# Optimization experiments

Measured on AMD Instinct MI355X. Metric: run time of the kernel, lower is better.

Reference implementation:

```python
import jax, jax.numpy as jnp
import numpy as np

B, H, W, A, C = 32, 64, 64, 5, 80
D = 5 + C  # per-anchor block


def setup_inputs() -> dict:
    key = jax.random.key(0)
    k1, k2, k3, k4 = jax.random.split(key, 4)
    model_output = jax.random.normal(k1, (B, H, W, A * D), jnp.float32) * 0.1
    # label: coords/classes in [0,1), wh offsets small, conf channel strictly 0 or 1
    lab = jax.random.uniform(k2, (B, H, W, A, D), jnp.float32)
    conf = (jax.random.uniform(k3, (B, H, W, A)) < 0.05).astype(jnp.float32)
    wh = jax.random.normal(k4, (B, H, W, A, 2), jnp.float32) * 0.3
    lab = lab.at[..., 2:4].set(wh).at[..., 4].set(conf)
    label = lab.reshape(B, H, W, A * D)
    original_img_sizes = jnp.full((B, 2), 416.0, jnp.float32)  # [h, w] per image
    anchor_boxes = jnp.array([[30.0, 25.0], [60.0, 55.0], [110.0, 95.0],
                              [180.0, 160.0], [300.0, 280.0]], jnp.float32)  # [A,2] = [h,w]
    return {"model_output": model_output, "label": label,
            "original_img_sizes": original_img_sizes, "anchor_boxes": anchor_boxes}


def _smooth_l1(x):
    ax = jnp.abs(x)
    return jnp.where(ax < 1.0, 0.5 * x * x, ax - 0.5)


def _yolo_loss(model_output, label, original_img_sizes, anchor_boxes,
               lamda_coord, lamda_noobj, lamda_obj, lamda_class):
    b, h, w, ch = model_output.shape
    a = anchor_boxes.shape[0]
    d = ch // a
    out = model_output.reshape(b, h, w, a, d)
    lab = label.reshape(b, h, w, a, d)

    obj = lab[..., 4] >= 1.0            # [B,H,W,A]
    noobj = lab[..., 4] == 0.0
    objf = obj.astype(out.dtype)
    noobjf = noobj.astype(out.dtype)

    xg = jnp.arange(w, dtype=out.dtype)[None, None, :, None]   # x grid index
    yg = jnp.arange(h, dtype=out.dtype)[None, :, None, None]   # y grid index
    ylen = (original_img_sizes[:, 0] / h)[:, None, None, None]
    xlen = (original_img_sizes[:, 1] / w)[:, None, None, None]
    aw = anchor_boxes[:, 1]  # broadcast over A axis
    ah = anchor_boxes[:, 0]

    # predicted box decode (NB: pred ymax uses x_center -- faithful to source bug)
    pxc = (xg + out[..., 0]) * xlen
    pyc = (yg + out[..., 1]) * ylen
    pw = jnp.exp(out[..., 2]) * aw
    ph = jnp.exp(out[..., 3]) * ah
    pxmin, pxmax = pxc - pw / 2, pxc + pw / 2
    pymin, pymax = pyc - ph / 2, pxc + ph / 2  # source bug: x_center here

    # true box decode
    txc = (xg + lab[..., 0]) * xlen
    tyc = (yg + lab[..., 1]) * ylen
    tw = jnp.exp(lab[..., 2]) * aw
    th = jnp.exp(lab[..., 3]) * ah
    txmin, txmax = txc - tw / 2, txc + tw / 2
    tymin, tymax = tyc - th / 2, tyc + th / 2

    iw = jnp.maximum(jnp.minimum(pxmax, txmax) - jnp.maximum(pxmin, txmin), 0.0)
    ih = jnp.maximum(jnp.minimum(pymax, tymax) - jnp.maximum(pymin, tymin), 0.0)
    inter = iw * ih
    area_p = (pxmax - pxmin) * (pymax - pymin)
    area_t = (txmax - txmin) * (tymax - tymin)
    union = area_p + area_t - inter
    iou = inter / jnp.where(obj, union, 1.0)
    iou = jnp.where(obj, iou, 0.0)      # ious tensor is zero at non-obj cells

    new_conf = lab[..., 4] * iou        # label conf channel *= ious

    p1 = (objf * ((out[..., :2] - lab[..., :2]) ** 2).sum(-1)).sum()
    p2 = (objf * _smooth_l1(out[..., 2:4] - lab[..., 2:4]).sum(-1)).sum()
    p3 = (objf * (out[..., 4] - new_conf) ** 2).sum()
    p4 = (noobjf * (out[..., 4] - new_conf) ** 2).sum()
    p5 = (objf * ((out[..., 5:] - lab[..., 5:]) ** 2).sum(-1)).sum()

    return (lamda_coord * p1 + lamda_coord * p2 + lamda_obj * p3
            + lamda_noobj * p4 + lamda_class * p5)


def reference(model_output, label, original_img_sizes, anchor_boxes,
              lamda_coord=5.0, lamda_noobj=0.5, lamda_obj=1.0, lamda_class=1.0):
    return _yolo_loss(model_output, label, original_img_sizes, anchor_boxes,
                      lamda_coord, lamda_noobj, lamda_obj, lamda_class)
```

## Files before the change

### kernel.cpp

```cpp
#include <hip/hip_runtime.h>


constexpr int Bc = 32, Hc = 64, Wc = 64, Ac = 5, Dc = 85, Cc = 80;
constexpr int NCELL = Bc * Hc * Wc * Ac;
constexpr float LAMDA_COORD = 5.0f;
constexpr float LAMDA_NOOBJ = 0.5f;
constexpr float LAMDA_OBJ   = 1.0f;
constexpr float LAMDA_CLASS = 1.0f;

__global__ void zero_kernel(float* out) {
    if (threadIdx.x == 0 && blockIdx.x == 0) out[0] = 0.0f;
}

__device__ __forceinline__ float smooth_l1(float x) {
    float ax = fabsf(x);
    return (ax < 1.0f) ? 0.5f * x * x : ax - 0.5f;
}

__global__ __launch_bounds__(256) void yolo_loss_kernel(
    const float* __restrict__ mo,
    const float* __restrict__ lb,
    const float* __restrict__ orig,
    const float* __restrict__ anch,
    float* __restrict__ result)
{
    int idx = blockIdx.x * blockDim.x + threadIdx.x;
    float loss = 0.0f;

    if (idx < NCELL) {
        long base = (long)idx * Dc;
        float lab4 = lb[base + 4];
        float out4 = mo[base + 4];

        if (lab4 == 0.0f) {
            loss = LAMDA_NOOBJ * out4 * out4;
        } else if (lab4 >= 1.0f) {
            int a = idx % Ac;
            int t = idx / Ac;
            int w = t % Wc; t /= Wc;
            int h = t % Hc;
            int b = t / Hc;

            float o0 = mo[base + 0], o1 = mo[base + 1];
            float o2 = mo[base + 2], o3 = mo[base + 3];
            float l0 = lb[base + 0], l1 = lb[base + 1];
            float l2 = lb[base + 2], l3 = lb[base + 3];

            float ylen = orig[b * 2 + 0] * (1.0f / Hc);
            float xlen = orig[b * 2 + 1] * (1.0f / Wc);
            float aw = anch[a * 2 + 1];
            float ah = anch[a * 2 + 0];

            float pxc = ((float)w + o0) * xlen;
            float pyc = ((float)h + o1) * ylen;
            float pw  = __expf(o2) * aw;
            float ph  = __expf(o3) * ah;
            float pxmin = pxc - pw * 0.5f, pxmax = pxc + pw * 0.5f;
            float pymin = pyc - ph * 0.5f;
            float pymax = pxc + ph * 0.5f;

            float txc = ((float)w + l0) * xlen;
            float tyc = ((float)h + l1) * ylen;
            float tw  = __expf(l2) * aw;
            float th  = __expf(l3) * ah;
            float txmin = txc - tw * 0.5f, txmax = txc + tw * 0.5f;
            float tymin = tyc - th * 0.5f, tymax = tyc + th * 0.5f;

            float iw = fmaxf(fminf(pxmax, txmax) - fmaxf(pxmin, txmin), 0.0f);
            float ih = fmaxf(fminf(pymax, tymax) - fmaxf(pymin, tymin), 0.0f);
            float inter  = iw * ih;
            float area_p = (pxmax - pxmin) * (pymax - pymin);
            float area_t = (txmax - txmin) * (tymax - tymin);
            float uni    = area_p + area_t - inter;
            float iou    = inter / uni;
            float new_conf = lab4 * iou;

            float d0 = o0 - l0, d1 = o1 - l1;
            float p1 = d0 * d0 + d1 * d1;
            float p2 = smooth_l1(o2 - l2) + smooth_l1(o3 - l3);
            float dc = out4 - new_conf;
            float p3 = dc * dc;

            float p5 = 0.0f;
            #pragma unroll 8
            for (int c = 0; c < Cc; ++c) {
                float d = mo[base + 5 + c] - lb[base + 5 + c];
                p5 += d * d;
            }

            loss = LAMDA_COORD * (p1 + p2) + LAMDA_OBJ * p3 + LAMDA_CLASS * p5;
        }
    }

    #pragma unroll
    for (int off = 32; off > 0; off >>= 1)
        loss += __shfl_down(loss, off);

    __shared__ float smem[4];
    int lane = threadIdx.x & 63;
    int wid  = threadIdx.x >> 6;
    if (lane == 0) smem[wid] = loss;
    __syncthreads();
    if (threadIdx.x == 0) {
        float tot = smem[0] + smem[1] + smem[2] + smem[3];
        atomicAdd(result, tot);
    }
}

extern "C" void kernel_launch(void* const* d_in, const int* in_sizes, int n_in,
                              void* d_out, int out_size, void* d_ws, size_t ws_size,
                              hipStream_t stream) {
    const float* mo   = (const float*)d_in[0];
    const float* lb   = (const float*)d_in[1];
    const float* orig = (const float*)d_in[2];
    const float* anch = (const float*)d_in[3];
    float* result = (float*)d_out;

    zero_kernel<<<1, 64, 0, stream>>>(result);

    int block = 256;
    int grid = (NCELL + block - 1) / block;
    yolo_loss_kernel<<<grid, block, 0, stream>>>(mo, lb, orig, anch, result);
}
```

Measured before the change: 60.69 us.

## Compact object cells in shared memory and process each with a full wavefront

Each thread now only checks the confidence channel and handles the no-object case itself. Object cells are appended to a shared-memory list, and each wavefront then handles one listed cell at a time: lanes load the 85 channels in a coalesced way, and the class loss is reduced with shuffles. This replaces strided per-thread loops over 80 class channels, which are uncoalesced and divergent, at the cost of extra barriers, a shared atomic, and shuffle reductions.

```diff
diff --git a/kernel.cpp b/kernel.cpp
--- a/kernel.cpp
+++ b/kernel.cpp
@@ -1,7 +1,7 @@
 #include <hip/hip_runtime.h>
 
 
-constexpr int Bc = 32, Hc = 64, Wc = 64, Ac = 5, Dc = 85, Cc = 80;
+constexpr int Bc = 32, Hc = 64, Wc = 64, Ac = 5, Dc = 85;
 constexpr int NCELL = Bc * Hc * Wc * Ac;
 constexpr float LAMDA_COORD = 5.0f;
 constexpr float LAMDA_NOOBJ = 0.5f;
@@ -24,85 +24,109 @@
     const float* __restrict__ anch,
     float* __restrict__ result)
 {
-    int idx = blockIdx.x * blockDim.x + threadIdx.x;
+    const int tid  = threadIdx.x;
+    const int lane = tid & 63;
+    const int wid  = tid >> 6;
+    const int idx  = blockIdx.x * 256 + tid;
+
+    __shared__ int   s_objidx[256];
+    __shared__ int   s_cnt;
+    __shared__ float s_partial[4];
+    if (tid == 0) s_cnt = 0;
+    __syncthreads();
+
     float loss = 0.0f;
 
-    if (idx < NCELL) {
+    {
         long base = (long)idx * Dc;
         float lab4 = lb[base + 4];
         float out4 = mo[base + 4];
-
         if (lab4 == 0.0f) {
             loss = LAMDA_NOOBJ * out4 * out4;
         } else if (lab4 >= 1.0f) {
-            int a = idx % Ac;
-            int t = idx / Ac;
-            int w = t % Wc; t /= Wc;
-            int h = t % Hc;
-            int b = t / Hc;
+            int p = atomicAdd(&s_cnt, 1);
+            s_objidx[p] = idx;
+        }
+    }
+    __syncthreads();
+    const int n = s_cnt;
 
-            float o0 = mo[base + 0], o1 = mo[base + 1];
-            float o2 = mo[base + 2], o3 = mo[base + 3];
-            float l0 = lb[base + 0], l1 = lb[base + 1];
-            float l2 = lb[base + 2], l3 = lb[base + 3];
+    for (int i = wid; i < n; i += 4) {
+        const int cidx = s_objidx[i];
+        const long base = (long)cidx * Dc;
 
-            float ylen = orig[b * 2 + 0] * (1.0f / Hc);
-            float xlen = orig[b * 2 + 1] * (1.0f / Wc);
-            float aw = anch[a * 2 + 1];
-            float ah = anch[a * 2 + 0];
+        float o_a = mo[base + lane];
+        float l_a = lb[base + lane];
+        float o_b = 0.0f, l_b = 0.0f;
+        if (lane < Dc - 64) {
+            o_b = mo[base + 64 + lane];
+            l_b = lb[base + 64 + lane];
+        }
 
-            float pxc = ((float)w + o0) * xlen;
-            float pyc = ((float)h + o1) * ylen;
-            float pw  = __expf(o2) * aw;
-            float ph  = __expf(o3) * ah;
-            float pxmin = pxc - pw * 0.5f, pxmax = pxc + pw * 0.5f;
-            float pymin = pyc - ph * 0.5f;
-            float pymax = pxc + ph * 0.5f;
+        float da = (lane >= 5) ? (o_a - l_a) : 0.0f;
+        float db = o_b - l_b;
+        float p5 = da * da + db * db;
+        #pragma unroll
+        for (int off = 32; off > 0; off >>= 1)
+            p5 += __shfl_down(p5, off);
 
-            float txc = ((float)w + l0) * xlen;
-            float tyc = ((float)h + l1) * ylen;
-            float tw  = __expf(l2) * aw;
-            float th  = __expf(l3) * ah;
-            float txmin = txc - tw * 0.5f, txmax = txc + tw * 0.5f;
-            float tymin = tyc - th * 0.5f, tymax = tyc + th * 0.5f;
+        float o0 = __shfl(o_a, 0), o1 = __shfl(o_a, 1), o2 = __shfl(o_a, 2),
+              o3 = __shfl(o_a, 3), o4 = __shfl(o_a, 4);
+        float l0 = __shfl(l_a, 0), l1 = __shfl(l_a, 1), l2 = __shfl(l_a, 2),
+              l3 = __shfl(l_a, 3), l4 = __shfl(l_a, 4);
 
-            float iw = fmaxf(fminf(pxmax, txmax) - fmaxf(pxmin, txmin), 0.0f);
-            float ih = fmaxf(fminf(pymax, tymax) - fmaxf(pymin, tymin), 0.0f);
-            float inter  = iw * ih;
-            float area_p = (pxmax - pxmin) * (pymax - pymin);
-            float area_t = (txmax - txmin) * (tymax - tymin);
-            float uni    = area_p + area_t - inter;
-            float iou    = inter / uni;
-            float new_conf = lab4 * iou;
+        int a = cidx % Ac;
+        int t = cidx / Ac;
+        int w = t & (Wc - 1); t >>= 6;
+        int h = t & (Hc - 1);
+        int b = t >> 6;
 
-            float d0 = o0 - l0, d1 = o1 - l1;
-            float p1 = d0 * d0 + d1 * d1;
-            float p2 = smooth_l1(o2 - l2) + smooth_l1(o3 - l3);
-            float dc = out4 - new_conf;
-            float p3 = dc * dc;
+        float ylen = orig[b * 2 + 0] * (1.0f / Hc);
+        float xlen = orig[b * 2 + 1] * (1.0f / Wc);
+        float aw = anch[a * 2 + 1];
+        float ah = anch[a * 2 + 0];
 
-            float p5 = 0.0f;
-            #pragma unroll 8
-            for (int c = 0; c < Cc; ++c) {
-                float d = mo[base + 5 + c] - lb[base + 5 + c];
-                p5 += d * d;
-            }
+        float pxc = ((float)w + o0) * xlen;
+        float pyc = ((float)h + o1) * ylen;
+        float pw  = __expf(o2) * aw;
+        float ph  = __expf(o3) * ah;
+        float pxmin = pxc - pw * 0.5f, pxmax = pxc + pw * 0.5f;
+        float pymin = pyc - ph * 0.5f;
+        float pymax = pxc + ph * 0.5f;
 
-            loss = LAMDA_COORD * (p1 + p2) + LAMDA_OBJ * p3 + LAMDA_CLASS * p5;
-        }
+        float txc = ((float)w + l0) * xlen;
+        float tyc = ((float)h + l1) * ylen;
+        float tw  = __expf(l2) * aw;
+        float th  = __expf(l3) * ah;
+        float txmin = txc - tw * 0.5f, txmax = txc + tw * 0.5f;
+        float tymin = tyc - th * 0.5f, tymax = tyc + th * 0.5f;
+
+        float iw = fmaxf(fminf(pxmax, txmax) - fmaxf(pxmin, txmin), 0.0f);
+        float ih = fmaxf(fminf(pymax, tymax) - fmaxf(pymin, tymin), 0.0f);
+        float inter  = iw * ih;
+        float area_p = (pxmax - pxmin) * (pymax - pymin);
+        float area_t = (txmax - txmin) * (tymax - tymin);
+        float uni    = area_p + area_t - inter;
+        float iou    = inter / uni;
+        float new_conf = l4 * iou;
+
+        float d0 = o0 - l0, d1 = o1 - l1;
+        float p1 = d0 * d0 + d1 * d1;
+        float p2 = smooth_l1(o2 - l2) + smooth_l1(o3 - l3);
+        float dc = o4 - new_conf;
+        float p3 = dc * dc;
+
+        if (lane == 0)
+            loss += LAMDA_COORD * (p1 + p2) + LAMDA_OBJ * p3 + LAMDA_CLASS * p5;
     }
 
     #pragma unroll
     for (int off = 32; off > 0; off >>= 1)
         loss += __shfl_down(loss, off);
-
-    __shared__ float smem[4];
-    int lane = threadIdx.x & 63;
-    int wid  = threadIdx.x >> 6;
-    if (lane == 0) smem[wid] = loss;
+    if (lane == 0) s_partial[wid] = loss;
     __syncthreads();
-    if (threadIdx.x == 0) {
-        float tot = smem[0] + smem[1] + smem[2] + smem[3];
+    if (tid == 0) {
+        float tot = s_partial[0] + s_partial[1] + s_partial[2] + s_partial[3];
         atomicAdd(result, tot);
     }
 }
@@ -119,6 +143,6 @@
     zero_kernel<<<1, 64, 0, stream>>>(result);
 
     int block = 256;
-    int grid = (NCELL + block - 1) / block;
+    int grid = NCELL / block;
     yolo_loss_kernel<<<grid, block, 0, stream>>>(mo, lb, orig, anch, result);
 }
```

Result: slower. 62.61 us (+3.2%).
